# Kernel tuning notes

Hardware: AMD Instinct MI355X
Metric: run time of the kernel (lower is better)

The kernel has to match this reference:

```python
import jax, jax.numpy as jnp
import numpy as np

POOL = 7        # pool_size
NUM_ROIS = 128  # num_rois
WINDOW = 4      # window_size


def setup_inputs() -> dict:
    key = jax.random.key(0)
    k1, k2 = jax.random.split(key)
    img = jax.random.normal(k1, (16, 28, 28, 512), dtype=jnp.float32)
    rois = jax.random.uniform(k2, (16, NUM_ROIS * 5), dtype=jnp.float32)
    return {"img": img, "rois": rois}


def _crop_and_resize(image, boxes, crop):
    """tf.image.crop_and_resize (bilinear, extrapolation_value=0) on a single image.
    image: (H, W, C); boxes: (N, 4) normalized (y1, x1, y2, x2). Returns (N, crop, crop, C)."""
    H, W, C = image.shape
    dt = image.dtype
    y1, x1, y2, x2 = boxes[:, 0], boxes[:, 1], boxes[:, 2], boxes[:, 3]
    i = jnp.arange(crop, dtype=dt)
    # sample grid (crop > 1 branch of TF crop_and_resize)
    ys = y1[:, None] * (H - 1) + i[None, :] * ((y2 - y1) * (H - 1) / (crop - 1))[:, None]  # (N, crop)
    xs = x1[:, None] * (W - 1) + i[None, :] * ((x2 - x1) * (W - 1) / (crop - 1))[:, None]  # (N, crop)
    y0f = jnp.floor(ys)
    x0f = jnp.floor(xs)
    ly = ys - y0f  # fractional weights
    lx = xs - x0f
    y0 = jnp.clip(y0f, 0, H - 1).astype(jnp.int32)
    y1i = jnp.clip(y0f + 1, 0, H - 1).astype(jnp.int32)
    x0 = jnp.clip(x0f, 0, W - 1).astype(jnp.int32)
    x1i = jnp.clip(x0f + 1, 0, W - 1).astype(jnp.int32)
    g = lambda yi, xi: image[yi[:, :, None], xi[:, None, :], :]  # (N, crop, crop, C) gather
    tl, tr, bl, br = g(y0, x0), g(y0, x1i), g(y1i, x0), g(y1i, x1i)
    lxb = lx[:, None, :, None]
    lyb = ly[:, :, None, None]
    val = (tl + (tr - tl) * lxb) * (1 - lyb) + (bl + (br - bl) * lxb) * lyb
    # out-of-range samples -> extrapolation_value = 0
    vy = (ys >= 0) & (ys <= H - 1)
    vx = (xs >= 0) & (xs <= W - 1)
    mask = (vy[:, :, None, None] & vx[:, None, :, None]).astype(dt)
    return val * mask


def reference(img, rois):
    B, H, W, C = img.shape  # H=W=28, C=512 per the layer's hardcoded reshape
    r = rois.reshape(-1, 5)[:, 3:]  # (B*num_rois, 2): columns 3,4 -> x1, y1
    x1 = r[:, 0]
    y1 = r[:, 1]
    x2 = x1 + WINDOW / W  # window_size / cols
    y2 = y1 + WINDOW / H  # window_size / rows
    boxes = jnp.stack([y1, x1, y2, x2], axis=-1)  # (B*num_rois, 4)
    # Original tiles img num_rois times but sets box_ind = zeros, so every crop
    # samples from batch element 0's feature map. Reproduce that exactly.
    crops = _crop_and_resize(img[0], boxes, POOL)  # (B*num_rois, POOL, POOL, C)
    return crops.reshape(B, POOL, POOL, NUM_ROIS * C)
```

## Files before the change

### kernel.cpp

```cpp
#include <hip/hip_runtime.h>

#define POOLSZ 7
#define NROIS  128
#define IMG_H  28
#define IMG_W  28
#define IMG_C  512
#define WINDOW 4
#define TOT_ROIS 2048
#define C4 (IMG_C / 4)
#define TOT_POS (TOT_ROIS * POOLSZ * POOLSZ)

typedef float f4 __attribute__((ext_vector_type(4)));

__global__ __launch_bounds__(256)
void roi_crop_resize_kernel(const float* __restrict__ img,
                            const float* __restrict__ rois,
                            float* __restrict__ out) {
    int t = blockIdx.x * 256 + threadIdx.x;
    int c4  = t & (C4 - 1);
    int pos = t >> 7;
    if (pos >= TOT_POS) return;

    int px  = pos % POOLSZ;
    int tmp = pos / POOLSZ;
    int py  = tmp % POOLSZ;
    int n   = tmp / POOLSZ;

    float x1 = rois[n * 5 + 3];
    float y1 = rois[n * 5 + 4];
    float x2 = x1 + (float)WINDOW / (float)IMG_W;
    float y2 = y1 + (float)WINDOW / (float)IMG_H;

    const float Hm1 = (float)(IMG_H - 1);
    const float Wm1 = (float)(IMG_W - 1);
    float ys = y1 * Hm1 + (float)py * ((y2 - y1) * Hm1 / (float)(POOLSZ - 1));
    float xs = x1 * Wm1 + (float)px * ((x2 - x1) * Wm1 / (float)(POOLSZ - 1));

    float y0f = floorf(ys);
    float x0f = floorf(xs);
    float ly = ys - y0f;
    float lx = xs - x0f;

    int y0  = (int)fminf(fmaxf(y0f,       0.f), Hm1);
    int y1i = (int)fminf(fmaxf(y0f + 1.f, 0.f), Hm1);
    int x0  = (int)fminf(fmaxf(x0f,       0.f), Wm1);
    int x1i = (int)fminf(fmaxf(x0f + 1.f, 0.f), Wm1);

    float m = ((ys >= 0.f) & (ys <= Hm1) & (xs >= 0.f) & (xs <= Wm1)) ? 1.f : 0.f;

    const f4* img4 = (const f4*)img;
    f4 tl = img4[(y0  * IMG_W + x0 ) * C4 + c4];
    f4 tr = img4[(y0  * IMG_W + x1i) * C4 + c4];
    f4 bl = img4[(y1i * IMG_W + x0 ) * C4 + c4];
    f4 br = img4[(y1i * IMG_W + x1i) * C4 + c4];

    float omly = 1.f - ly;
    f4 v = ((tl + (tr - tl) * lx) * omly + (bl + (br - bl) * lx) * ly) * m;

    __builtin_nontemporal_store(v, ((f4*)out) + pos * C4 + c4);
}

extern "C" void kernel_launch(void* const* d_in, const int* in_sizes, int n_in,
                              void* d_out, int out_size, void* d_ws, size_t ws_size,
                              hipStream_t stream) {
    const float* img  = (const float*)d_in[0];
    const float* rois = (const float*)d_in[1];
    float* out = (float*)d_out;

    long long total = (long long)TOT_POS * C4;
    int grid = (int)((total + 255) / 256);
    roi_crop_resize_kernel<<<grid, 256, 0, stream>>>(img, rois, out);
}
```

Before: 239.2 us.

## Stage per-ROI image patch in LDS and interpolate from shared memory

Each block now handles one ROI and a quarter of the channels. It first loads a 6x6 pixel patch around the ROI into LDS, then computes all 49 bilinear samples from LDS instead of four global gathers per output. This is meant to cut redundant L2/global reads of the image. In exchange it adds a barrier per block and a per-block patch load that may not amortize well.

```diff
diff --git a/kernel.cpp b/kernel.cpp
--- a/kernel.cpp
+++ b/kernel.cpp
@@ -1,63 +1,80 @@
 #include <hip/hip_runtime.h>
 
 #define POOLSZ 7
-#define NROIS  128
 #define IMG_H  28
 #define IMG_W  28
 #define IMG_C  512
-#define WINDOW 4
+#define C4     128
+#define SLICES 4
+#define SC4    (C4 / SLICES)
 #define TOT_ROIS 2048
-#define C4 (IMG_C / 4)
-#define TOT_POS (TOT_ROIS * POOLSZ * POOLSZ)
+#define PATCH  6
 
 typedef float f4 __attribute__((ext_vector_type(4)));
 
 __global__ __launch_bounds__(256)
-void roi_crop_resize_kernel(const float* __restrict__ img,
-                            const float* __restrict__ rois,
-                            float* __restrict__ out) {
-    int t = blockIdx.x * 256 + threadIdx.x;
-    int c4  = t & (C4 - 1);
-    int pos = t >> 7;
-    if (pos >= TOT_POS) return;
+void roi_crop_resize_lds(const float* __restrict__ img,
+                         const float* __restrict__ rois,
+                         float* __restrict__ out) {
+    __shared__ f4 lds[PATCH * PATCH * SC4];
 
-    int px  = pos % POOLSZ;
-    int tmp = pos / POOLSZ;
-    int py  = tmp % POOLSZ;
-    int n   = tmp / POOLSZ;
+    int n     = blockIdx.x >> 2;
+    int slice = blockIdx.x & 3;
 
     float x1 = rois[n * 5 + 3];
     float y1 = rois[n * 5 + 4];
-    float x2 = x1 + (float)WINDOW / (float)IMG_W;
-    float y2 = y1 + (float)WINDOW / (float)IMG_H;
+    float x2 = x1 + 4.0f / 28.0f;
+    float y2 = y1 + 4.0f / 28.0f;
+    const float Hm1 = 27.0f, Wm1 = 27.0f;
+    float dy  = (y2 - y1) * Hm1 / 6.0f;
+    float dx  = (x2 - x1) * Wm1 / 6.0f;
+    float ys0 = y1 * Hm1;
+    float xs0 = x1 * Wm1;
 
-    const float Hm1 = (float)(IMG_H - 1);
-    const float Wm1 = (float)(IMG_W - 1);
-    float ys = y1 * Hm1 + (float)py * ((y2 - y1) * Hm1 / (float)(POOLSZ - 1));
-    float xs = x1 * Wm1 + (float)px * ((x2 - x1) * Wm1 / (float)(POOLSZ - 1));
-
-    float y0f = floorf(ys);
-    float x0f = floorf(xs);
-    float ly = ys - y0f;
-    float lx = xs - x0f;
-
-    int y0  = (int)fminf(fmaxf(y0f,       0.f), Hm1);
-    int y1i = (int)fminf(fmaxf(y0f + 1.f, 0.f), Hm1);
-    int x0  = (int)fminf(fmaxf(x0f,       0.f), Wm1);
-    int x1i = (int)fminf(fmaxf(x0f + 1.f, 0.f), Wm1);
-
-    float m = ((ys >= 0.f) & (ys <= Hm1) & (xs >= 0.f) & (xs <= Wm1)) ? 1.f : 0.f;
+    int Y0 = (int)floorf(ys0); if (Y0 > 27) Y0 = 27; if (Y0 < 0) Y0 = 0;
+    int X0 = (int)floorf(xs0); if (X0 > 27) X0 = 27; if (X0 < 0) X0 = 0;
 
     const f4* img4 = (const f4*)img;
-    f4 tl = img4[(y0  * IMG_W + x0 ) * C4 + c4];
-    f4 tr = img4[(y0  * IMG_W + x1i) * C4 + c4];
-    f4 bl = img4[(y1i * IMG_W + x0 ) * C4 + c4];
-    f4 br = img4[(y1i * IMG_W + x1i) * C4 + c4];
+    int tid = threadIdx.x;
 
-    float omly = 1.f - ly;
-    f4 v = ((tl + (tr - tl) * lx) * omly + (bl + (br - bl) * lx) * ly) * m;
+    for (int i = tid; i < PATCH * PATCH * SC4; i += 256) {
+        int c   = i & (SC4 - 1);
+        int pix = i >> 5;
+        int ry  = Y0 + pix / PATCH; if (ry > 27) ry = 27;
+        int rx  = X0 + pix % PATCH; if (rx > 27) rx = 27;
+        lds[i] = img4[(ry * IMG_W + rx) * C4 + slice * SC4 + c];
+    }
+    __syncthreads();
 
-    __builtin_nontemporal_store(v, ((f4*)out) + pos * C4 + c4);
+    f4* out4 = (f4*)out;
+    for (int i = tid; i < 49 * SC4; i += 256) {
+        int c  = i & (SC4 - 1);
+        int p  = i >> 5;
+        int py = p / POOLSZ, px = p % POOLSZ;
+
+        float ys = ys0 + (float)py * dy;
+        float xs = xs0 + (float)px * dx;
+        float y0f = floorf(ys), x0f = floorf(xs);
+        float ly = ys - y0f, lx = xs - x0f;
+        int y0  = (int)fminf(fmaxf(y0f,       0.f), Hm1);
+        int y1i = (int)fminf(fmaxf(y0f + 1.f, 0.f), Hm1);
+        int x0  = (int)fminf(fmaxf(x0f,       0.f), Wm1);
+        int x1i = (int)fminf(fmaxf(x0f + 1.f, 0.f), Wm1);
+        float m = ((ys >= 0.f) & (ys <= Hm1) & (xs >= 0.f) & (xs <= Wm1)) ? 1.f : 0.f;
+
+        int ry0 = y0  - Y0, ry1 = y1i - Y0;
+        int rx0 = x0  - X0, rx1 = x1i - X0;
+        f4 tl = lds[(ry0 * PATCH + rx0) * SC4 + c];
+        f4 tr = lds[(ry0 * PATCH + rx1) * SC4 + c];
+        f4 bl = lds[(ry1 * PATCH + rx0) * SC4 + c];
+        f4 br = lds[(ry1 * PATCH + rx1) * SC4 + c];
+
+        float omly = 1.f - ly;
+        f4 v = ((tl + (tr - tl) * lx) * omly + (bl + (br - bl) * lx) * ly) * m;
+
+        int pos = n * 49 + p;
+        __builtin_nontemporal_store(v, out4 + pos * C4 + slice * SC4 + c);
+    }
 }
 
 extern "C" void kernel_launch(void* const* d_in, const int* in_sizes, int n_in,
@@ -67,7 +84,5 @@
     const float* rois = (const float*)d_in[1];
     float* out = (float*)d_out;
 
-    long long total = (long long)TOT_POS * C4;
-    int grid = (int)((total + 255) / 256);
-    roi_crop_resize_kernel<<<grid, 256, 0, stream>>>(img, rois, out);
+    roi_crop_resize_lds<<<TOT_ROIS * SLICES, 256, 0, stream>>>(img, rois, out);
 }
```

Measured after the change: 216.8 us. 9.4% less time.
